# Kernel optimization log

Hardware: AMD Instinct MI355X
Metric: run time of the kernel (lower is better)

Reference implementation:

```python
import jax, jax.numpy as jnp
import numpy as np

N, M = 32768, 1024

def setup_inputs() -> dict:
    key = jax.random.key(0)
    k1, k2, k3, k4, k5 = jax.random.split(key, 5)
    origins = jax.random.normal(k1, (N, 2), dtype=jnp.float32)
    directions = jax.random.normal(k2, (N, 2), dtype=jnp.float32)
    means = jax.random.normal(k3, (M, 4), dtype=jnp.float32)
    # SPD covariances: A @ A^T + I so the inverse is well-defined
    A = jax.random.normal(k4, (M, 4, 4), dtype=jnp.float32) * 0.5
    covariances = jnp.einsum('mij,mkj->mik', A, A) + jnp.eye(4, dtype=jnp.float32)
    labels_embedding = jax.random.normal(k5, (M,), dtype=jnp.float32)
    return {"origins": origins, "directions": directions, "means": means,
            "covariances": covariances, "labels_embedding": labels_embedding}

def reference(origins, directions, means, covariances, labels_embedding):
    pos = jnp.concatenate([origins, directions], axis=1)          # [N,4]
    Sigma_inv = jnp.linalg.inv(covariances)                       # [M,4,4]
    diffs = pos[:, None, :] - means[None, :, :]                   # [N,M,4]
    quad = jnp.einsum('nmd,mde,nme->nm', diffs, Sigma_inv, diffs)  # [N,M]
    pdf = jnp.exp(-0.5 * quad) * labels_embedding[None, :]        # [N,M]
    prob = jax.nn.sigmoid(jnp.sum(pdf, axis=1))                   # [N]
    return prob.reshape(-1, 1)
```

## Files before the change

kernel.cpp:

```cpp
#include <hip/hip_runtime.h>
#include <hip/hip_bf16.h>
#include <math.h>

#define N_RAYS  32768
#define M_GAUSS 1024

typedef short v8s __attribute__((ext_vector_type(8)));
typedef float v4f __attribute__((ext_vector_type(4)));

__device__ __forceinline__ float fexp2(float x) {
#if __has_builtin(__builtin_amdgcn_exp2f)
    return __builtin_amdgcn_exp2f(x);
#else
    return exp2f(x);
#endif
}

union BFU { __hip_bfloat16 b; unsigned short u; };
__device__ __forceinline__ unsigned short f2bf(float f) { BFU x; x.b = __float2bfloat16(f); return x.u; }
__device__ __forceinline__ float bf2f(unsigned short u)  { BFU x; x.u = u; return __bfloat162float(x.b); }

__device__ __forceinline__ void split_bf16(float f, unsigned short& hi, unsigned short& lo) {
    hi = f2bf(f);
    lo = f2bf(f - bf2f(hi));
}

__device__ __forceinline__ void store8(unsigned short* dst, const unsigned short* s) {
    uint4 v;
    v.x = (unsigned)s[0] | ((unsigned)s[1] << 16);
    v.y = (unsigned)s[2] | ((unsigned)s[3] << 16);
    v.z = (unsigned)s[4] | ((unsigned)s[5] << 16);
    v.w = (unsigned)s[6] | ((unsigned)s[7] << 16);
    *reinterpret_cast<uint4*>(dst) = v;
}

__global__ __launch_bounds__(256) void prep_kernel(
    const float2* __restrict__ org,
    const float2* __restrict__ dir,
    const float*  __restrict__ means,
    const float*  __restrict__ covs,
    unsigned short* __restrict__ Fs,
    unsigned short* __restrict__ Bt)
{
    const int n = blockIdx.x * 256 + threadIdx.x;

    {
        const float2 o = org[n];
        const float2 d = dir[n];
        const float p0 = o.x, p1 = o.y, p2 = d.x, p3 = d.y;
        float f[16] = { p0*p0, p1*p1, p2*p2, p3*p3,
                        p0*p1, p0*p2, p0*p3, p1*p2, p1*p3, p2*p3,
                        p0, p1, p2, p3, 1.0f, 0.0f };
        unsigned short hi[16], lo[16];
        #pragma unroll
        for (int k = 0; k < 16; ++k) split_bf16(f[k], hi[k], lo[k]);

        const int rt = n >> 4, c = n & 15;
        unsigned short* base = Fs + (size_t)rt * 64 * 8;
        store8(base + (0*16 + c) * 8, hi + 0);
        store8(base + (1*16 + c) * 8, hi + 8);
        store8(base + (2*16 + c) * 8, lo + 0);
        store8(base + (3*16 + c) * 8, lo + 8);
    }

    if (n < M_GAUSS) {
        const int g = n;
        const float4* C4 = reinterpret_cast<const float4*>(covs + 16 * g);
        const float4 r0 = C4[0], r1 = C4[1], r2 = C4[2], r3 = C4[3];
        const float a00=r0.x, a01=r0.y, a02=r0.z, a03=r0.w;
        const float a10=r1.x, a11=r1.y, a12=r1.z, a13=r1.w;
        const float a20=r2.x, a21=r2.y, a22=r2.z, a23=r2.w;
        const float a30=r3.x, a31=r3.y, a32=r3.z, a33=r3.w;

        const float s0=a00*a11-a01*a10, s1=a00*a12-a02*a10, s2=a00*a13-a03*a10;
        const float s3=a01*a12-a02*a11, s4=a01*a13-a03*a11, s5=a02*a13-a03*a12;
        const float c5=a22*a33-a23*a32, c4=a21*a33-a23*a31, c3=a21*a32-a22*a31;
        const float c2=a20*a33-a23*a30, c1=a20*a32-a22*a30, c0=a20*a31-a21*a30;
        const float det = s0*c5 - s1*c4 + s2*c3 + s3*c2 - s4*c1 + s5*c0;
        const float id  = 1.0f / det;

        const float b00=( a11*c5 - a12*c4 + a13*c3)*id;
        const float b01=(-a01*c5 + a02*c4 - a03*c3)*id;
        const float b10=(-a10*c5 + a12*c2 - a13*c1)*id;
        const float b11=( a00*c5 - a02*c2 + a03*c1)*id;
        const float b20=( a10*c4 - a11*c2 + a13*c0)*id;
        const float b21=(-a00*c4 + a01*c2 - a03*c0)*id;
        const float b30=(-a10*c3 + a11*c1 - a12*c0)*id;
        const float b31=( a00*c3 - a01*c1 + a02*c0)*id;
        const float b02=( a31*s5 - a32*s4 + a33*s3)*id;
        const float b03=(-a21*s5 + a22*s4 - a23*s3)*id;
        const float b12=(-a30*s5 + a32*s2 - a33*s1)*id;
        const float b13=( a20*s5 - a22*s2 + a23*s1)*id;
        const float b22=( a30*s4 - a31*s2 + a33*s0)*id;
        const float b23=(-a20*s4 + a21*s2 - a23*s0)*id;
        const float b32=(-a30*s3 + a31*s1 - a32*s0)*id;
        const float b33=( a20*s3 - a21*s1 + a22*s0)*id;

        const float m01=0.5f*(b01+b10), m02=0.5f*(b02+b20), m03=0.5f*(b03+b30);
        const float m12=0.5f*(b12+b21), m13=0.5f*(b13+b31), m23=0.5f*(b23+b32);

        const float4 mu = reinterpret_cast<const float4*>(means)[g];
        const float u0=mu.x, u1=mu.y, u2=mu.z, u3=mu.w;
        const float v0 = b00*u0 + m01*u1 + m02*u2 + m03*u3;
        const float v1 = m01*u0 + b11*u1 + m12*u2 + m13*u3;
        const float v2 = m02*u0 + m12*u1 + b22*u2 + m23*u3;
        const float v3 = m03*u0 + m13*u1 + m23*u2 + b33*u3;
        const float cc = u0*v0 + u1*v1 + u2*v2 + u3*v3;

        const float k  = -0.72134752044448170368f;
        const float k2 = 2.0f * k;
        float w[16] = { k*b00,  k*b11,  k*b22,  k*b33,
                        k2*m01, k2*m02, k2*m03, k2*m12, k2*m13, k2*m23,
                        -k2*v0, -k2*v1, -k2*v2, -k2*v3, k*cc, 0.0f };
        unsigned short whi[16], wlo[16];
        #pragma unroll
        for (int q = 0; q < 16; ++q) split_bf16(w[q], whi[q], wlo[q]);

        const int t = g >> 4, cg = g & 15;
        unsigned short* b1 = Bt + (size_t)t * 32 * 8;
        store8(b1 + (0*16 + cg) * 8, whi + 0);
        store8(b1 + (1*16 + cg) * 8, whi + 8);
        unsigned short* b2 = Bt + (size_t)2048 * 8 + (size_t)t * 32 * 8;
        store8(b2 + (0*16 + cg) * 8, wlo + 0);
        store8(b2 + (1*16 + cg) * 8, wlo + 8);
    }
}

__global__ __launch_bounds__(512) void decoder_kernel(
    const uint4* __restrict__ Fs,
    const uint4* __restrict__ Btg,
    const float* __restrict__ labels,
    float*       __restrict__ out)
{
    __shared__ uint4 lds[4096];

    const int tid = threadIdx.x;
    const int L   = tid & 63;
    const int w   = tid >> 6;
    const int c15 = L & 15;
    const int q   = L >> 4;

    #pragma unroll
    for (int i = 0; i < 8; ++i) lds[i * 512 + tid] = Btg[i * 512 + tid];

    const int rt0 = blockIdx.x * 4;
    v8s af[4];
    #pragma unroll
    for (int rt = 0; rt < 4; ++rt) {
        union { uint4 u; v8s s; } x;
        x.u = Fs[(size_t)(rt0 + rt) * 64 + L];
        af[rt] = x.s;
    }
    __syncthreads();

    v4f acc[4];
    #pragma unroll
    for (int rt = 0; rt < 4; ++rt) acc[rt] = (v4f){0.f, 0.f, 0.f, 0.f};

    const bool loHalf = (L < 32);
    #pragma unroll
    for (int i = 0; i < 8; ++i) {
        const int t = w * 8 + i;
        union { uint4 u; v8s s; } b1x, b2x;
        b1x.u = lds[t * 32 + (L & 31)];
        uint4 b2u = lds[2048 + t * 32 + (L & 31)];
        if (!loHalf) { b2u.x = 0; b2u.y = 0; b2u.z = 0; b2u.w = 0; }
        b2x.u = b2u;
        const float lab = labels[t * 16 + c15];

        #pragma unroll
        for (int rt = 0; rt < 4; ++rt) {
            v4f cz = (v4f){0.f, 0.f, 0.f, 0.f};
            v4f s = __builtin_amdgcn_mfma_f32_16x16x32_bf16(af[rt], b2x.s, cz, 0, 0, 0);
            s = __builtin_amdgcn_mfma_f32_16x16x32_bf16(af[rt], b1x.s, s, 0, 0, 0);
            #pragma unroll
            for (int r = 0; r < 4; ++r)
                acc[rt][r] = fmaf(lab, fexp2(s[r]), acc[rt][r]);
        }
    }

    __syncthreads();
    float* P = reinterpret_cast<float*>(lds);
    #pragma unroll
    for (int rt = 0; rt < 4; ++rt) {
        #pragma unroll
        for (int r = 0; r < 4; ++r) {
            const int ray = rt * 16 + q * 4 + r;
            P[(w << 10) + (ray << 4) + c15] = acc[rt][r];
        }
    }
    __syncthreads();

    if (tid < 64) {
        float tsum = 0.f;
        #pragma unroll
        for (int wv = 0; wv < 8; ++wv) {
            const float4* row = reinterpret_cast<const float4*>(P + (wv << 10) + (tid << 4));
            #pragma unroll
            for (int c4 = 0; c4 < 4; ++c4) {
                const float4 v = row[c4];
                tsum += (v.x + v.y) + (v.z + v.w);
            }
        }
        const float e = fexp2(-tsum * 1.4426950408889634f);
        out[blockIdx.x * 64 + tid] = 1.0f / (1.0f + e);
    }
}

extern "C" void kernel_launch(void* const* d_in, const int* in_sizes, int n_in,
                              void* d_out, int out_size, void* d_ws, size_t ws_size,
                              hipStream_t stream) {
    const float* origins    = (const float*)d_in[0];
    const float* directions = (const float*)d_in[1];
    const float* means      = (const float*)d_in[2];
    const float* covs       = (const float*)d_in[3];
    const float* labels     = (const float*)d_in[4];
    float* out = (float*)d_out;

    char* ws = (char*)d_ws;
    unsigned short* Fs = (unsigned short*)ws;
    unsigned short* Bt = (unsigned short*)(ws + (size_t)2 * 1024 * 1024);

    prep_kernel<<<dim3(N_RAYS / 256), dim3(256), 0, stream>>>(
        (const float2*)origins, (const float2*)directions, means, covs, Fs, Bt);
    decoder_kernel<<<dim3(N_RAYS / 64), dim3(512), 0, stream>>>(
        (const uint4*)Fs, (const uint4*)Bt, labels, out);
}
```

Before: 70.56 us.

## Fuse ray feature construction into decoder kernel via shared memory

Moves the per-ray quadratic feature build and bf16 hi/lo split out of the prep kernel and into the decoder. Each block's first wave now writes the feature tiles straight into shared memory. The prep kernel shrinks to the 1024 Gaussians (4 blocks instead of 128), and the global Fs workspace round-trip of about 4 MB is removed. The cost is that the first wave does extra work before the barrier, and the block uses 4 KB more shared memory.

```diff
diff --git a/kernel.cpp b/kernel.cpp
--- a/kernel.cpp
+++ b/kernel.cpp
@@ -35,18 +35,95 @@
 }
 
 __global__ __launch_bounds__(256) void prep_kernel(
+    const float*  __restrict__ means,
+    const float*  __restrict__ covs,
+    unsigned short* __restrict__ Bt)
+{
+    const int g = blockIdx.x * 256 + threadIdx.x;
+    if (g >= M_GAUSS) return;
+
+    const float4* C4 = reinterpret_cast<const float4*>(covs + 16 * g);
+    const float4 r0 = C4[0], r1 = C4[1], r2 = C4[2], r3 = C4[3];
+    const float a00=r0.x, a01=r0.y, a02=r0.z, a03=r0.w;
+    const float a10=r1.x, a11=r1.y, a12=r1.z, a13=r1.w;
+    const float a20=r2.x, a21=r2.y, a22=r2.z, a23=r2.w;
+    const float a30=r3.x, a31=r3.y, a32=r3.z, a33=r3.w;
+
+    const float s0=a00*a11-a01*a10, s1=a00*a12-a02*a10, s2=a00*a13-a03*a10;
+    const float s3=a01*a12-a02*a11, s4=a01*a13-a03*a11, s5=a02*a13-a03*a12;
+    const float c5=a22*a33-a23*a32, c4=a21*a33-a23*a31, c3=a21*a32-a22*a31;
+    const float c2=a20*a33-a23*a30, c1=a20*a32-a22*a30, c0=a20*a31-a21*a30;
+    const float det = s0*c5 - s1*c4 + s2*c3 + s3*c2 - s4*c1 + s5*c0;
+    const float id  = 1.0f / det;
+
+    const float b00=( a11*c5 - a12*c4 + a13*c3)*id;
+    const float b01=(-a01*c5 + a02*c4 - a03*c3)*id;
+    const float b10=(-a10*c5 + a12*c2 - a13*c1)*id;
+    const float b11=( a00*c5 - a02*c2 + a03*c1)*id;
+    const float b20=( a10*c4 - a11*c2 + a13*c0)*id;
+    const float b21=(-a00*c4 + a01*c2 - a03*c0)*id;
+    const float b30=(-a10*c3 + a11*c1 - a12*c0)*id;
+    const float b31=( a00*c3 - a01*c1 + a02*c0)*id;
+    const float b02=( a31*s5 - a32*s4 + a33*s3)*id;
+    const float b03=(-a21*s5 + a22*s4 - a23*s3)*id;
+    const float b12=(-a30*s5 + a32*s2 - a33*s1)*id;
+    const float b13=( a20*s5 - a22*s2 + a23*s1)*id;
+    const float b22=( a30*s4 - a31*s2 + a33*s0)*id;
+    const float b23=(-a20*s4 + a21*s2 - a23*s0)*id;
+    const float b32=(-a30*s3 + a31*s1 - a32*s0)*id;
+    const float b33=( a20*s3 - a21*s1 + a22*s0)*id;
+
+    const float m01=0.5f*(b01+b10), m02=0.5f*(b02+b20), m03=0.5f*(b03+b30);
+    const float m12=0.5f*(b12+b21), m13=0.5f*(b13+b31), m23=0.5f*(b23+b32);
+
+    const float4 mu = reinterpret_cast<const float4*>(means)[g];
+    const float u0=mu.x, u1=mu.y, u2=mu.z, u3=mu.w;
+    const float v0 = b00*u0 + m01*u1 + m02*u2 + m03*u3;
+    const float v1 = m01*u0 + b11*u1 + m12*u2 + m13*u3;
+    const float v2 = m02*u0 + m12*u1 + b22*u2 + m23*u3;
+    const float v3 = m03*u0 + m13*u1 + m23*u2 + b33*u3;
+    const float cc = u0*v0 + u1*v1 + u2*v2 + u3*v3;
+
+    const float k  = -0.72134752044448170368f;
+    const float k2 = 2.0f * k;
+    float w[16] = { k*b00,  k*b11,  k*b22,  k*b33,
+                    k2*m01, k2*m02, k2*m03, k2*m12, k2*m13, k2*m23,
+                    -k2*v0, -k2*v1, -k2*v2, -k2*v3, k*cc, 0.0f };
+    unsigned short whi[16], wlo[16];
+    #pragma unroll
+    for (int q = 0; q < 16; ++q) split_bf16(w[q], whi[q], wlo[q]);
+
+    const int t = g >> 4, cg = g & 15;
+    unsigned short* b1 = Bt + (size_t)t * 32 * 8;
+    store8(b1 + (0*16 + cg) * 8, whi + 0);
+    store8(b1 + (1*16 + cg) * 8, whi + 8);
+    unsigned short* b2 = Bt + (size_t)2048 * 8 + (size_t)t * 32 * 8;
+    store8(b2 + (0*16 + cg) * 8, wlo + 0);
+    store8(b2 + (1*16 + cg) * 8, wlo + 8);
+}
+
+__global__ __launch_bounds__(512) void decoder_kernel(
     const float2* __restrict__ org,
     const float2* __restrict__ dir,
-    const float*  __restrict__ means,
-    const float*  __restrict__ covs,
-    unsigned short* __restrict__ Fs,
-    unsigned short* __restrict__ Bt)
+    const uint4* __restrict__ Btg,
+    const float* __restrict__ labels,
+    float*       __restrict__ out)
 {
-    const int n = blockIdx.x * 256 + threadIdx.x;
-
-    {
-        const float2 o = org[n];
-        const float2 d = dir[n];
+    __shared__ uint4 lds[4096 + 256];
+
+    const int tid = threadIdx.x;
+    const int L   = tid & 63;
+    const int w   = tid >> 6;
+    const int c15 = L & 15;
+    const int q   = L >> 4;
+
+    #pragma unroll
+    for (int i = 0; i < 8; ++i) lds[i * 512 + tid] = Btg[i * 512 + tid];
+
+    if (tid < 64) {
+        const int ray = blockIdx.x * 64 + tid;
+        const float2 o = org[ray];
+        const float2 d = dir[ray];
         const float p0 = o.x, p1 = o.y, p2 = d.x, p3 = d.y;
         float f[16] = { p0*p0, p1*p1, p2*p2, p3*p3,
                         p0*p1, p0*p2, p0*p3, p1*p2, p1*p3, p2*p3,
@@ -55,103 +132,23 @@
         #pragma unroll
         for (int k = 0; k < 16; ++k) split_bf16(f[k], hi[k], lo[k]);
 
-        const int rt = n >> 4, c = n & 15;
-        unsigned short* base = Fs + (size_t)rt * 64 * 8;
+        unsigned short* At = reinterpret_cast<unsigned short*>(lds + 4096);
+        const int rt = tid >> 4, c = tid & 15;
+        unsigned short* base = At + rt * 64 * 8;
         store8(base + (0*16 + c) * 8, hi + 0);
         store8(base + (1*16 + c) * 8, hi + 8);
         store8(base + (2*16 + c) * 8, lo + 0);
         store8(base + (3*16 + c) * 8, lo + 8);
     }
-
-    if (n < M_GAUSS) {
-        const int g = n;
-        const float4* C4 = reinterpret_cast<const float4*>(covs + 16 * g);
-        const float4 r0 = C4[0], r1 = C4[1], r2 = C4[2], r3 = C4[3];
-        const float a00=r0.x, a01=r0.y, a02=r0.z, a03=r0.w;
-        const float a10=r1.x, a11=r1.y, a12=r1.z, a13=r1.w;
-        const float a20=r2.x, a21=r2.y, a22=r2.z, a23=r2.w;
-        const float a30=r3.x, a31=r3.y, a32=r3.z, a33=r3.w;
-
-        const float s0=a00*a11-a01*a10, s1=a00*a12-a02*a10, s2=a00*a13-a03*a10;
-        const float s3=a01*a12-a02*a11, s4=a01*a13-a03*a11, s5=a02*a13-a03*a12;
-        const float c5=a22*a33-a23*a32, c4=a21*a33-a23*a31, c3=a21*a32-a22*a31;
-        const float c2=a20*a33-a23*a30, c1=a20*a32-a22*a30, c0=a20*a31-a21*a30;
-        const float det = s0*c5 - s1*c4 + s2*c3 + s3*c2 - s4*c1 + s5*c0;
-        const float id  = 1.0f / det;
-
-        const float b00=( a11*c5 - a12*c4 + a13*c3)*id;
-        const float b01=(-a01*c5 + a02*c4 - a03*c3)*id;
-        const float b10=(-a10*c5 + a12*c2 - a13*c1)*id;
-        const float b11=( a00*c5 - a02*c2 + a03*c1)*id;
-        const float b20=( a10*c4 - a11*c2 + a13*c0)*id;
-        const float b21=(-a00*c4 + a01*c2 - a03*c0)*id;
-        const float b30=(-a10*c3 + a11*c1 - a12*c0)*id;
-        const float b31=( a00*c3 - a01*c1 + a02*c0)*id;
-        const float b02=( a31*s5 - a32*s4 + a33*s3)*id;
-        const float b03=(-a21*s5 + a22*s4 - a23*s3)*id;
-        const float b12=(-a30*s5 + a32*s2 - a33*s1)*id;
-        const float b13=( a20*s5 - a22*s2 + a23*s1)*id;
-        const float b22=( a30*s4 - a31*s2 + a33*s0)*id;
-        const float b23=(-a20*s4 + a21*s2 - a23*s0)*id;
-        const float b32=(-a30*s3 + a31*s1 - a32*s0)*id;
-        const float b33=( a20*s3 - a21*s1 + a22*s0)*id;
-
-        const float m01=0.5f*(b01+b10), m02=0.5f*(b02+b20), m03=0.5f*(b03+b30);
-        const float m12=0.5f*(b12+b21), m13=0.5f*(b13+b31), m23=0.5f*(b23+b32);
-
-        const float4 mu = reinterpret_cast<const float4*>(means)[g];
-        const float u0=mu.x, u1=mu.y, u2=mu.z, u3=mu.w;
-        const float v0 = b00*u0 + m01*u1 + m02*u2 + m03*u3;
-        const float v1 = m01*u0 + b11*u1 + m12*u2 + m13*u3;
-        const float v2 = m02*u0 + m12*u1 + b22*u2 + m23*u3;
-        const float v3 = m03*u0 + m13*u1 + m23*u2 + b33*u3;
-        const float cc = u0*v0 + u1*v1 + u2*v2 + u3*v3;
-
-        const float k  = -0.72134752044448170368f;
-        const float k2 = 2.0f * k;
-        float w[16] = { k*b00,  k*b11,  k*b22,  k*b33,
-                        k2*m01, k2*m02, k2*m03, k2*m12, k2*m13, k2*m23,
-                        -k2*v0, -k2*v1, -k2*v2, -k2*v3, k*cc, 0.0f };
-        unsigned short whi[16], wlo[16];
-        #pragma unroll
-        for (int q = 0; q < 16; ++q) split_bf16(w[q], whi[q], wlo[q]);
-
-        const int t = g >> 4, cg = g & 15;
-        unsigned short* b1 = Bt + (size_t)t * 32 * 8;
-        store8(b1 + (0*16 + cg) * 8, whi + 0);
-        store8(b1 + (1*16 + cg) * 8, whi + 8);
-        unsigned short* b2 = Bt + (size_t)2048 * 8 + (size_t)t * 32 * 8;
-        store8(b2 + (0*16 + cg) * 8, wlo + 0);
-        store8(b2 + (1*16 + cg) * 8, wlo + 8);
-    }
-}
-
-__global__ __launch_bounds__(512) void decoder_kernel(
-    const uint4* __restrict__ Fs,
-    const uint4* __restrict__ Btg,
-    const float* __restrict__ labels,
-    float*       __restrict__ out)
-{
-    __shared__ uint4 lds[4096];
-
-    const int tid = threadIdx.x;
-    const int L   = tid & 63;
-    const int w   = tid >> 6;
-    const int c15 = L & 15;
-    const int q   = L >> 4;
-
-    #pragma unroll
-    for (int i = 0; i < 8; ++i) lds[i * 512 + tid] = Btg[i * 512 + tid];
-
-    const int rt0 = blockIdx.x * 4;
+    __syncthreads();
+
     v8s af[4];
     #pragma unroll
     for (int rt = 0; rt < 4; ++rt) {
         union { uint4 u; v8s s; } x;
-        x.u = Fs[(size_t)(rt0 + rt) * 64 + L];
+        x.u = lds[4096 + rt * 64 + L];
         af[rt] = x.s;
     }
-    __syncthreads();
 
     v4f acc[4];
     #pragma unroll
@@ -217,12 +214,10 @@
     const float* labels     = (const float*)d_in[4];
     float* out = (float*)d_out;
 
-    char* ws = (char*)d_ws;
-    unsigned short* Fs = (unsigned short*)ws;
-    unsigned short* Bt = (unsigned short*)(ws + (size_t)2 * 1024 * 1024);
-
-    prep_kernel<<<dim3(N_RAYS / 256), dim3(256), 0, stream>>>(
-        (const float2*)origins, (const float2*)directions, means, covs, Fs, Bt);
+    unsigned short* Bt = (unsigned short*)d_ws;
+
+    prep_kernel<<<dim3(M_GAUSS / 256), dim3(256), 0, stream>>>(means, covs, Bt);
     decoder_kernel<<<dim3(N_RAYS / 64), dim3(512), 0, stream>>>(
-        (const uint4*)Fs, (const uint4*)Bt, labels, out);
-}
+        (const float2*)origins, (const float2*)directions,
+        (const uint4*)Bt, labels, out);
+}
```

Measured after the change: 69.90 us. No clear change (-0.9%).
